# Optimization experiments

Measured on AMD Instinct MI355X. Metric: run time of the kernel, lower is better.

## Reference

```python
import math
import jax, jax.numpy as jnp
import numpy as np

# dims (match init_kwargs / input_specs)
N_H = 16        # heads
N_I = 64        # number of intent slots appended to the key axis
N_B = 8         # buckets (one-hot has N_B+1 classes)
D_MODEL = 1024
D_K = D_MODEL // N_H
EPSILON = 0.25
TOP_K = int(N_I * EPSILON)   # = 16
BS = 2
MAXLEN = 1024
N2 = MAXLEN + N_I            # intent length = seq keys + intents


def setup_inputs() -> dict:
    key = jax.random.key(0)
    k0, k1, k2, k3, k4, k5 = jax.random.split(key, 6)
    item = jax.random.normal(k0, (BS, MAXLEN, D_MODEL), dtype=jnp.float32)
    intent = jax.random.normal(k1, (BS, N2, D_MODEL), dtype=jnp.float32)
    mask = jnp.ones((BS, 1, MAXLEN, N2), dtype=jnp.bool_)
    b_seq = jax.random.randint(k2, (BS, MAXLEN), 0, N_B + 1)
    b_seq2 = jax.random.randint(k3, (BS, N2), 0, N_B + 1)
    # learned params: [1, n_b+1, d_model, h, d_k] and [2, n_b+1, d_model, h, d_k]
    W_item = jax.random.normal(k4, (1, N_B + 1, D_MODEL, N_H, D_K), dtype=jnp.float32) * 0.02
    W_intent = jax.random.normal(k5, (2, N_B + 1, D_MODEL, N_H, D_K), dtype=jnp.float32) * 0.02
    return {"item": item, "intent": intent, "mask": mask,
            "b_seq": b_seq, "b_seq2": b_seq2,
            "W_item": W_item, "W_intent": W_intent}


def _rank_mask(x, k):
    # torch double-sort trick: True where element is NOT among the top-k of the row
    order = jnp.argsort(-x, axis=-1)          # descending sort indices (idx1)
    rank = jnp.argsort(order, axis=-1)        # rank of each position (idx2)
    return rank >= k


def reference(item, intent, mask, b_seq, b_seq2, W_item, W_intent):
    oh_q = jax.nn.one_hot(b_seq, N_B + 1, dtype=item.dtype)      # [b, n, B]
    oh_kv = jax.nn.one_hot(b_seq2, N_B + 1, dtype=intent.dtype)  # [b, m, B]
    # bucket-gated projections
    q = jnp.einsum('bnd,Bdhk,bnB->bhnk', item, W_item[0], oh_q)
    k = jnp.einsum('bmd,Bdhk,bmB->bhmk', intent, W_intent[0], oh_kv)
    v = jnp.einsum('bmd,Bdhk,bmB->bhmk', intent, W_intent[1], oh_kv)
    # attention scores [b, h, n, m]
    scores = jnp.einsum('bhnk,bhmk->bhnm', q, k) / math.sqrt(D_K)
    scores = jnp.where(mask, scores, jnp.float32(-1e30))
    p = jax.nn.softmax(scores, axis=-1)  # dropout = identity (eval reference)
    # split key axis: sequence part vs last n_i intents, top-k mask each part
    p_bs = p[..., :-N_I]
    p_ba = p[..., -N_I:]
    topk_mask = jnp.concatenate([_rank_mask(p_bs, TOP_K), _rank_mask(p_ba, TOP_K)], axis=-1)
    p_masked = jnp.where(topk_mask, jnp.float32(0.0), p)
    # 'belong' indices: argmax position per query row at head 0
    sIdx = jnp.argmax(p_bs[:, 0], axis=-1)[..., None]  # [b, n, 1]
    aIdx = jnp.argmax(p_ba[:, 0], axis=-1)[..., None]  # [b, n, 1]
    x = jnp.einsum('bhnm,bhmk->bhnk', p_masked, v)
    x = jnp.transpose(x, (0, 2, 1, 3)).reshape(BS, MAXLEN, N_H * D_K)
    return (x, sIdx, aIdx)
```

## Files before the change

### kernel.cpp

```cpp
#include <hip/hip_runtime.h>

#define NHEAD   16
#define DK      64
#define DMODEL  1024
#define BSZ     2
#define SEQLEN  1024
#define NI      64
#define NN2     1088
#define NBUCK   9
#define TOPK    16

#define T_ITEM  (BSZ*SEQLEN)
#define T_INT   (BSZ*NN2)

#define Q_OFF   ((size_t)0)
#define K_OFF   (Q_OFF + (size_t)T_ITEM*DMODEL*4)
#define V_OFF   (K_OFF + (size_t)T_INT*DMODEL*4)
#define QKV_BYTES (V_OFF + (size_t)T_INT*DMODEL*4)
#define CNT_OFF QKV_BYTES
#define LI_OFF  (CNT_OFF + 128)
#define LN_OFF  (LI_OFF + (size_t)NBUCK*T_ITEM*4)
#define WS_NEED (LN_OFF + (size_t)NBUCK*T_INT*4)
#define P_OFF   ((WS_NEED + 255) & ~(size_t)255)
#define WS_NEED2 (P_OFF + QKV_BYTES)

#define Q0D_OFF V_OFF
#define K0D_OFF (V_OFF + (size_t)T_ITEM*64*8)

#define X_OUT_ELEMS ((size_t)BSZ*SEQLEN*DMODEL)
#define SIDX_ELEMS  ((size_t)BSZ*SEQLEN)

__device__ __forceinline__ int clampi(int v, int lo, int hi) {
  return v < lo ? lo : (v > hi ? hi : v);
}

__global__ void bucketize_kernel(const int* __restrict__ b_seq, const int* __restrict__ b_seq2,
                                 int* __restrict__ cnt, int* __restrict__ list_item,
                                 int* __restrict__ list_int) {
  int t = blockIdx.x * blockDim.x + threadIdx.x;
  if (t < T_ITEM) {
    int B = clampi(b_seq[t], 0, NBUCK - 1);
    int p = atomicAdd(&cnt[B], 1);
    if (p >= 0 && p < T_ITEM) list_item[B * T_ITEM + p] = t;
  }
  if (t < T_INT) {
    int B = clampi(b_seq2[t], 0, NBUCK - 1);
    int p = atomicAdd(&cnt[NBUCK + B], 1);
    if (p >= 0 && p < T_INT) list_int[B * T_INT + p] = t;
  }
}

__global__ __launch_bounds__(256) void proj_head0_f64_v2(
    const float* __restrict__ item, const float* __restrict__ intent,
    const float* __restrict__ Wq, const float* __restrict__ Wk,
    const int* __restrict__ b_seq, const int* __restrict__ b_seq2,
    double* __restrict__ q0d, double* __restrict__ k0dT) {
  const int blk = blockIdx.x;
  const int wv = (int)threadIdx.x >> 6, lane = (int)threadIdx.x & 63;
  const float* X; const float* W; const int* bs; int tok; bool tr;
  if (blk < T_ITEM) { tok = blk;          X = item;   W = Wq; bs = b_seq;  tr = false; }
  else              { tok = blk - T_ITEM; X = intent; W = Wk; bs = b_seq2; tr = true; }
  const int B = clampi(bs[tok], 0, NBUCK - 1);
  const float* xr = X + (size_t)tok * DMODEL;
  const float* wb = W + (size_t)B * DMODEL * (NHEAD * DK) + lane;
  double acc = 0.0;
  const int d0 = wv * 256;
  #pragma unroll 8
  for (int d = d0; d < d0 + 256; ++d)
    acc += (double)xr[d] * (double)wb[(size_t)d * (NHEAD * DK)];
  __shared__ double part[4][64];
  part[wv][lane] = acc;
  __syncthreads();
  if (wv == 0) {
    double s = ((part[0][lane] + part[1][lane]) + part[2][lane]) + part[3][lane];
    if (tr) k0dT[(size_t)lane * T_INT + tok] = s;
    else    q0d[(size_t)tok * 64 + lane] = s;
  }
}

#define AR 4
__global__ __launch_bounds__(256) void argmax_f64_v2(
    const double* __restrict__ Q0, const double* __restrict__ K0T,
    float* __restrict__ out_s, float* __restrict__ out_a) {
  const int n0 = blockIdx.x * AR;
  const int b = n0 >> 10;
  const int t = (int)threadIdx.x;
  __shared__ double qs[AR][64];
  qs[t >> 6][t & 63] = Q0[(size_t)(n0 + (t >> 6)) * 64 + (t & 63)];
  __syncthreads();
  double v1[AR], v2[AR]; int i1[AR], i2[AR];
  #pragma unroll
  for (int r = 0; r < AR; ++r) {
    v1[r] = -1e300; i1[r] = 0x7FFFFFFF;
    v2[r] = -1e300; i2[r] = 0x7FFFFFFF;
  }
  for (int m = t; m < NN2; m += 256) {
    const double* base = K0T + (size_t)b * NN2 + m;
    double s0 = 0.0, s1 = 0.0, s2 = 0.0, s3 = 0.0;
    #pragma unroll 8
    for (int k = 0; k < 64; ++k) {
      const double kv = base[(size_t)k * T_INT];
      s0 += qs[0][k] * kv; s1 += qs[1][k] * kv;
      s2 += qs[2][k] * kv; s3 += qs[3][k] * kv;
    }
    const double ss[AR] = {s0, s1, s2, s3};
    #pragma unroll
    for (int r = 0; r < AR; ++r) {
      const double s = ss[r];
      if (m < 1024) { if (s > v1[r] || (s == v1[r] && m < i1[r])) { v1[r] = s; i1[r] = m; } }
      else          { if (s > v2[r] || (s == v2[r] && m < i2[r])) { v2[r] = s; i2[r] = m; } }
    }
  }
  __shared__ double bval[256];  __shared__ int bidx[256];
  __shared__ double bval2[256]; __shared__ int bidx2[256];
  for (int r = 0; r < AR; ++r) {
    __syncthreads();
    bval[t] = v1[r]; bidx[t] = i1[r]; bval2[t] = v2[r]; bidx2[t] = i2[r];
    __syncthreads();
    for (int off = 128; off >= 1; off >>= 1) {
      if (t < off) {
        if (bval[t+off] >  bval[t] || (bval[t+off] ==  bval[t] &&  bidx[t+off] <  bidx[t])) { bval[t]  = bval[t+off];  bidx[t]  = bidx[t+off]; }
        if (bval2[t+off] > bval2[t] || (bval2[t+off] == bval2[t] && bidx2[t+off] < bidx2[t])) { bval2[t] = bval2[t+off]; bidx2[t] = bidx2[t+off]; }
      }
      __syncthreads();
    }
    if (t == 0) {
      out_s[n0 + r] = (float)bidx[0];
      out_a[n0 + r] = (float)(bidx2[0] - 1024);
    }
  }
}

#define GTM 128
#define GTN 128
#define GBK 16

__global__ __launch_bounds__(256) void gemm_grouped_fused(
    const float* __restrict__ item, const float* __restrict__ intent,
    const float* __restrict__ Wq, const float* __restrict__ Wk,
    const float* __restrict__ Wv,
    const int* __restrict__ list_item, const int* __restrict__ list_int,
    const int* __restrict__ cnt,
    float* __restrict__ qb, float* __restrict__ kb, float* __restrict__ vb,
    float* __restrict__ pq, float* __restrict__ pk, float* __restrict__ pv,
    const int klen) {
  const int z = blockIdx.z;
  const int s = z / 27;
  const int rem = z - s * 27;
  const int g = rem / 9, B = rem - g * 9;
  const int kbeg = s * klen;
  const float* X;  const float* W;  const int* list;  float* Y;  int n, Tmax;
  if (g == 0)      { X = item;   W = Wq; list = list_item; Y = s ? pq : qb; n = min(cnt[B], T_ITEM);        Tmax = T_ITEM; }
  else if (g == 1) { X = intent; W = Wk; list = list_int;  Y = s ? pk : kb; n = min(cnt[NBUCK + B], T_INT); Tmax = T_INT; }
  else             { X = intent; W = Wv; list = list_int;  Y = s ? pv : vb; n = min(cnt[NBUCK + B], T_INT); Tmax = T_INT; }

  const int row0 = blockIdx.y * GTM;
  if (row0 >= n) return;
  const int rows = min(GTM, n - row0);
  const int c0 = blockIdx.x * GTN;
  const int t = (int)threadIdx.x;

  __shared__ float Xs[GBK][GTM + 4];
  __shared__ float Ws[GBK][GTN];

  const int tokA = t >> 1;
  const int kqA  = (t & 1) * 8;
  const int liA  = clampi(list[row0 + min(tokA, rows - 1)], 0, Tmax - 1);
  const float* xrow = X + (size_t)liA * DMODEL;
  const int kW  = t >> 4;
  const int cW  = (t & 15) * 4;
  const float* wbase = W + ((size_t)B * DMODEL + kW) * (size_t)(NHEAD * DK) + c0 + cW;

  const int ty = t >> 4;
  const int tx = t & 15;

  float acc[8][8];
  #pragma unroll
  for (int i = 0; i < 8; ++i)
    #pragma unroll
    for (int j = 0; j < 8; ++j) acc[i][j] = 0.f;

  float4 xa = *(const float4*)(xrow + kbeg + kqA);
  float4 xb = *(const float4*)(xrow + kbeg + kqA + 4);
  float4 wa = *(const float4*)(wbase + (size_t)kbeg * (NHEAD * DK));
  float4 wc = *(const float4*)(wbase + (size_t)kbeg * (NHEAD * DK) + 64);

  for (int k0 = kbeg; k0 < kbeg + klen; k0 += GBK) {
    __syncthreads();
    Xs[kqA + 0][tokA] = xa.x; Xs[kqA + 1][tokA] = xa.y;
    Xs[kqA + 2][tokA] = xa.z; Xs[kqA + 3][tokA] = xa.w;
    Xs[kqA + 4][tokA] = xb.x; Xs[kqA + 5][tokA] = xb.y;
    Xs[kqA + 6][tokA] = xb.z; Xs[kqA + 7][tokA] = xb.w;
    *(float4*)&Ws[kW][cW]      = wa;
    *(float4*)&Ws[kW][cW + 64] = wc;
    __syncthreads();

    if (k0 + GBK < kbeg + klen) {
      xa = *(const float4*)(xrow + k0 + GBK + kqA);
      xb = *(const float4*)(xrow + k0 + GBK + kqA + 4);
      wa = *(const float4*)(wbase + (size_t)(k0 + GBK) * (NHEAD * DK));
      wc = *(const float4*)(wbase + (size_t)(k0 + GBK) * (NHEAD * DK) + 64);
    }

    #pragma unroll
    for (int kk = 0; kk < GBK; ++kk) {
      float a[8], bv[8];
      *(float4*)&a[0]  = *(const float4*)&Xs[kk][ty * 8];
      *(float4*)&a[4]  = *(const float4*)&Xs[kk][ty * 8 + 4];
      *(float4*)&bv[0] = *(const float4*)&Ws[kk][tx * 4];
      *(float4*)&bv[4] = *(const float4*)&Ws[kk][tx * 4 + 64];
      #pragma unroll
      for (int i = 0; i < 8; ++i)
        #pragma unroll
        for (int j = 0; j < 8; ++j)
          acc[i][j] = fmaf(a[i], bv[j], acc[i][j]);
    }
  }

  #pragma unroll
  for (int i = 0; i < 8; ++i) {
    const int r = ty * 8 + i;
    if (r < rows) {
      const int tok = clampi(list[row0 + r], 0, Tmax - 1);
      float* yr = Y + (size_t)tok * (size_t)(NHEAD * DK) + c0 + tx * 4;
      *(float4*)yr        = make_float4(acc[i][0], acc[i][1], acc[i][2], acc[i][3]);
      *(float4*)(yr + 64) = make_float4(acc[i][4], acc[i][5], acc[i][6], acc[i][7]);
    }
  }
}

__global__ __launch_bounds__(256) void reduce_add(
    float4* __restrict__ y, const float4* __restrict__ p, const int n4) {
  const int stride = gridDim.x * blockDim.x;
  for (int i = blockIdx.x * blockDim.x + threadIdx.x; i < n4; i += stride) {
    float4 a = y[i]; const float4 b = p[i];
    a.x += b.x; a.y += b.y; a.z += b.z; a.w += b.w;
    y[i] = a;
  }
}

__device__ __forceinline__ unsigned ordf(float v) {
  unsigned s = __float_as_uint(v);
  return s ^ ((unsigned)((int)s >> 31) | 0x80000000u);
}
__device__ __forceinline__ float unordf(unsigned u) {
  unsigned s = (u & 0x80000000u) ? (u ^ 0x80000000u) : ~u;
  return __uint_as_float(s);
}
__device__ __forceinline__ unsigned long long shfl_xor_u64(unsigned long long w, int off) {
  unsigned lo = __shfl_xor((unsigned)w, off);
  unsigned hi = __shfl_xor((unsigned)(w >> 32), off);
  return ((unsigned long long)hi << 32) | lo;
}

__global__ __launch_bounds__(256) void attn_kernel(
    const float* __restrict__ Q, const float* __restrict__ K,
    const float* __restrict__ V, float* __restrict__ outx) {
  const int b = blockIdx.z, h = blockIdx.y;
  const int n0 = blockIdx.x * 16;
  const int t = (int)threadIdx.x;
  const int wave = t >> 6, lane = t & 63;

  __shared__ float Qs[16][64];
  __shared__ float Ks[192][68];
  __shared__ int   kept_m[16][32];
  __shared__ float kept_p[16][32];

  {
    const int r = t >> 4, k4 = (t & 15) * 4;
    *(float4*)&Qs[r][k4] =
        *(const float4*)(Q + (size_t)(b * SEQLEN + n0 + r) * (NHEAD * DK) + h * DK + k4);
  }
  __syncthreads();

  const int r0 = wave * 4;
  float sv[4][17];

  #pragma unroll
  for (int p = 0; p < 5; ++p) {
    if (p > 0) __syncthreads();
    #pragma unroll
    for (int j = 0; j < 12; ++j) {
      const int row = (t >> 4) + 16 * j;
      const int k4 = (t & 15) * 4;
      *(float4*)&Ks[row][k4] =
          *(const float4*)(K + (size_t)(b * NN2 + p * 192 + row) * (NHEAD * DK) + h * DK + k4);
    }
    __syncthreads();

    float a0[3], a1[3], a2[3], a3[3];
    #pragma unroll
    for (int c = 0; c < 3; ++c) { a0[c] = 0.f; a1[c] = 0.f; a2[c] = 0.f; a3[c] = 0.f; }
    #pragma unroll 4
    for (int k4 = 0; k4 < 64; k4 += 4) {
      float4 kc[3];
      kc[0] = *(const float4*)&Ks[lane][k4];
      kc[1] = *(const float4*)&Ks[64 + lane][k4];
      kc[2] = *(const float4*)&Ks[128 + lane][k4];
      const float4 q0 = *(const float4*)&Qs[r0 + 0][k4];
      const float4 q1 = *(const float4*)&Qs[r0 + 1][k4];
      const float4 q2 = *(const float4*)&Qs[r0 + 2][k4];
      const float4 q3 = *(const float4*)&Qs[r0 + 3][k4];
      #pragma unroll
      for (int c = 0; c < 3; ++c) {
        a0[c] = fmaf(q0.x, kc[c].x, a0[c]); a0[c] = fmaf(q0.y, kc[c].y, a0[c]);
        a0[c] = fmaf(q0.z, kc[c].z, a0[c]); a0[c] = fmaf(q0.w, kc[c].w, a0[c]);
        a1[c] = fmaf(q1.x, kc[c].x, a1[c]); a1[c] = fmaf(q1.y, kc[c].y, a1[c]);
        a1[c] = fmaf(q1.z, kc[c].z, a1[c]); a1[c] = fmaf(q1.w, kc[c].w, a1[c]);
        a2[c] = fmaf(q2.x, kc[c].x, a2[c]); a2[c] = fmaf(q2.y, kc[c].y, a2[c]);
        a2[c] = fmaf(q2.z, kc[c].z, a2[c]); a2[c] = fmaf(q2.w, kc[c].w, a2[c]);
        a3[c] = fmaf(q3.x, kc[c].x, a3[c]); a3[c] = fmaf(q3.y, kc[c].y, a3[c]);
        a3[c] = fmaf(q3.z, kc[c].z, a3[c]); a3[c] = fmaf(q3.w, kc[c].w, a3[c]);
      }
    }
    #pragma unroll
    for (int c = 0; c < 3; ++c) {
      sv[0][3 * p + c] = a0[c] * 0.125f; sv[1][3 * p + c] = a1[c] * 0.125f;
      sv[2][3 * p + c] = a2[c] * 0.125f; sv[3][3 * p + c] = a3[c] * 0.125f;
    }
  }

  {
    __syncthreads();
    #pragma unroll
    for (int j = 0; j < 8; ++j) {
      const int row = (t >> 4) + 16 * j;
      const int k4 = (t & 15) * 4;
      *(float4*)&Ks[row][k4] =
          *(const float4*)(K + (size_t)(b * NN2 + 960 + row) * (NHEAD * DK) + h * DK + k4);
    }
    __syncthreads();

    float a0[2], a1[2], a2[2], a3[2];
    #pragma unroll
    for (int c = 0; c < 2; ++c) { a0[c] = 0.f; a1[c] = 0.f; a2[c] = 0.f; a3[c] = 0.f; }
    #pragma unroll 4
    for (int k4 = 0; k4 < 64; k4 += 4) {
      float4 kc[2];
      kc[0] = *(const float4*)&Ks[lane][k4];
      kc[1] = *(const float4*)&Ks[64 + lane][k4];
      const float4 q0 = *(const float4*)&Qs[r0 + 0][k4];
      const float4 q1 = *(const float4*)&Qs[r0 + 1][k4];
      const float4 q2 = *(const float4*)&Qs[r0 + 2][k4];
      const float4 q3 = *(const float4*)&Qs[r0 + 3][k4];
      #pragma unroll
      for (int c = 0; c < 2; ++c) {
        a0[c] = fmaf(q0.x, kc[c].x, a0[c]); a0[c] = fmaf(q0.y, kc[c].y, a0[c]);
        a0[c] = fmaf(q0.z, kc[c].z, a0[c]); a0[c] = fmaf(q0.w, kc[c].w, a0[c]);
        a1[c] = fmaf(q1.x, kc[c].x, a1[c]); a1[c] = fmaf(q1.y, kc[c].y, a1[c]);
        a1[c] = fmaf(q1.z, kc[c].z, a1[c]); a1[c] = fmaf(q1.w, kc[c].w, a1[c]);
        a2[c] = fmaf(q2.x, kc[c].x, a2[c]); a2[c] = fmaf(q2.y, kc[c].y, a2[c]);
        a2[c] = fmaf(q2.z, kc[c].z, a2[c]); a2[c] = fmaf(q2.w, kc[c].w, a2[c]);
        a3[c] = fmaf(q3.x, kc[c].x, a3[c]); a3[c] = fmaf(q3.y, kc[c].y, a3[c]);
        a3[c] = fmaf(q3.z, kc[c].z, a3[c]); a3[c] = fmaf(q3.w, kc[c].w, a3[c]);
      }
    }
    #pragma unroll
    for (int c = 0; c < 2; ++c) {
      sv[0][15 + c] = a0[c] * 0.125f; sv[1][15 + c] = a1[c] * 0.125f;
      sv[2][15 + c] = a2[c] * 0.125f; sv[3][15 + c] = a3[c] * 0.125f;
    }
  }

  float M_[4], invL_[4];
  {
    float L_[4];
    #pragma unroll
    for (int r = 0; r < 4; ++r) {
      float M = -3.402823466e38f;
      #pragma unroll
      for (int c = 0; c < 17; ++c) M = fmaxf(M, sv[r][c]);
      M_[r] = M;
    }
    #pragma unroll
    for (int off = 32; off >= 1; off >>= 1) {
      #pragma unroll
      for (int r = 0; r < 4; ++r) M_[r] = fmaxf(M_[r], __shfl_xor(M_[r], off));
    }
    #pragma unroll
    for (int r = 0; r < 4; ++r) {
      float L = 0.f;
      #pragma unroll
      for (int c = 0; c < 17; ++c) L += __expf(sv[r][c] - M_[r]);
      L_[r] = L;
    }
    #pragma unroll
    for (int off = 32; off >= 1; off >>= 1) {
      #pragma unroll
      for (int r = 0; r < 4; ++r) L_[r] += __shfl_xor(L_[r], off);
    }
    #pragma unroll
    for (int r = 0; r < 4; ++r) invL_[r] = 1.0f / L_[r];
  }

  unsigned kh[4][16];
  #pragma unroll
  for (int r = 0; r < 4; ++r)
    #pragma unroll
    for (int c = 0; c < 16; ++c) kh[r][c] = ordf(sv[r][c]);

  unsigned long long b1_[4], b2_[4];
  unsigned alive_[4];
  #pragma unroll
  for (int r = 0; r < 4; ++r) {
    unsigned long long b1 = 0ull, b2 = 0ull;
    #pragma unroll
    for (int c = 0; c < 16; ++c) {
      const unsigned long long k64 =
          ((unsigned long long)kh[r][c] << 32) | (unsigned)~(unsigned)(c * 64 + lane);
      const unsigned long long mn = (k64 < b1) ? k64 : b1;
      b1 = (k64 > b1) ? k64 : b1;
      b2 = (mn > b2) ? mn : b2;
    }
    b1_[r] = b1; b2_[r] = b2; alive_[r] = 0xFFFFu;
  }

  for (int round = 0; round < TOPK; ++round) {
    unsigned long long w0 = b1_[0], w1 = b1_[1], w2 = b1_[2], w3 = b1_[3];
    #pragma unroll
    for (int off = 1; off < 64; off <<= 1) {
      unsigned long long o;
      o = shfl_xor_u64(w0, off); w0 = (o > w0) ? o : w0;
      o = shfl_xor_u64(w1, off); w1 = (o > w1) ? o : w1;
      o = shfl_xor_u64(w2, off); w2 = (o > w2) ? o : w2;
      o = shfl_xor_u64(w3, off); w3 = (o > w3) ? o : w3;
    }
    const unsigned long long ws[4] = {w0, w1, w2, w3};
    #pragma unroll
    for (int r = 0; r < 4; ++r) {
      const unsigned long long w = ws[r];
      const int m = (int)((~(unsigned)w) & 1023u);
      if (lane == round) {
        kept_m[r0 + r][round] = m;
        kept_p[r0 + r][round] = __expf(unordf((unsigned)(w >> 32)) - M_[r]) * invL_[r];
      }
      if ((m & 63) == lane) {
        alive_[r] &= ~(1u << (m >> 6));
        if (b2_[r]) { b1_[r] = b2_[r]; b2_[r] = 0ull; }
        else {
          unsigned long long mx = 0ull;
          #pragma unroll
          for (int c = 0; c < 16; ++c) {
            const unsigned long long k64 =
                ((unsigned long long)kh[r][c] << 32) | (unsigned)~(unsigned)(c * 64 + lane);
            if ((alive_[r] >> c) & 1u) mx = (k64 > mx) ? k64 : mx;
          }
          b1_[r] = mx;
        }
      }
    }
  }

  {
    unsigned long long w_[4];
    #pragma unroll
    for (int r = 0; r < 4; ++r)
      w_[r] = ((unsigned long long)ordf(sv[r][16]) << 32) | (unsigned)~(unsigned)lane;
    #pragma unroll
    for (int k = 2; k <= 64; k <<= 1) {
      #pragma unroll
      for (int j = k >> 1; j >= 1; j >>= 1) {
        const bool tm = (((lane & j) != 0) == ((lane & k) != 0));
        #pragma unroll
        for (int r = 0; r < 4; ++r) {
          const unsigned long long o = shfl_xor_u64(w_[r], j);
          w_[r] = ((o > w_[r]) == tm) ? o : w_[r];
        }
      }
    }
    if (lane < TOPK) {
      #pragma unroll
      for (int r = 0; r < 4; ++r) {
        kept_m[r0 + r][TOPK + lane] = 1024 + (int)((~(unsigned)w_[r]) & 63u);
        kept_p[r0 + r][TOPK + lane] =
            __expf(unordf((unsigned)(w_[r] >> 32)) - M_[r]) * invL_[r];
      }
    }
  }
  __syncthreads();

  #pragma unroll
  for (int rr = 0; rr < 4; ++rr) {
    const int r_loc = wave * 4 + rr;
    const int n = n0 + r_loc;
    float x = 0.f;
    #pragma unroll
    for (int i = 0; i < 32; ++i) {
      const int m = clampi(kept_m[r_loc][i], 0, NN2 - 1);
      const float p = kept_p[r_loc][i];
      x = fmaf(p, V[(size_t)(b * NN2 + m) * (NHEAD * DK) + h * DK + lane], x);
    }
    outx[(size_t)(b * SEQLEN + n) * (NHEAD * DK) + h * DK + lane] = x;
  }
}

extern "C" void kernel_launch(void* const* d_in, const int* in_sizes, int n_in,
                              void* d_out, int out_size, void* d_ws, size_t ws_size,
                              hipStream_t stream) {
  const float* item    = (const float*)d_in[0];
  const float* intent  = (const float*)d_in[1];
  const int*   b_seq   = (const int*)d_in[3];
  const int*   b_seq2  = (const int*)d_in[4];
  const float* W_item  = (const float*)d_in[5];
  const float* W_int   = (const float*)d_in[6];

  if (ws_size < WS_NEED) return;

  char* ws = (char*)d_ws;
  float* qb = (float*)(ws + Q_OFF);
  float* kb = (float*)(ws + K_OFF);
  float* vb = (float*)(ws + V_OFF);
  double* q0d = (double*)(ws + Q0D_OFF);
  double* k0dT = (double*)(ws + K0D_OFF);
  int* cnt       = (int*)(ws + CNT_OFF);
  int* list_item = (int*)(ws + LI_OFF);
  int* list_int  = (int*)(ws + LN_OFF);

  const bool sk = (ws_size >= WS_NEED2);
  float* pq = sk ? (float*)(ws + P_OFF + Q_OFF) : qb;
  float* pk = sk ? (float*)(ws + P_OFF + K_OFF) : kb;
  float* pv = sk ? (float*)(ws + P_OFF + V_OFF) : vb;

  float* outx  = (float*)d_out;
  float* out_s = outx + X_OUT_ELEMS;
  float* out_a = out_s + SIDX_ELEMS;

  hipMemsetAsync(cnt, 0, 128, stream);
  bucketize_kernel<<<dim3(9), 256, 0, stream>>>(b_seq, b_seq2, cnt, list_item, list_int);

  proj_head0_f64_v2<<<dim3(T_ITEM + T_INT), 256, 0, stream>>>(
      item, intent, W_item, W_int, b_seq, b_seq2, q0d, k0dT);
  argmax_f64_v2<<<dim3(T_ITEM / AR), 256, 0, stream>>>(q0d, k0dT, out_s, out_a);

  const int klen = sk ? (DMODEL / 2) : DMODEL;
  const int nz   = sk ? 54 : 27;
  gemm_grouped_fused<<<dim3((NHEAD * DK) / GTN, 17, nz), 256, 0, stream>>>(
      item, intent,
      W_item, W_int, W_int + (size_t)NBUCK * DMODEL * (NHEAD * DK),
      list_item, list_int, cnt, qb, kb, vb, pq, pk, pv, klen);
  if (sk) {
    reduce_add<<<dim3(2048), 256, 0, stream>>>(
        (float4*)(ws + Q_OFF), (float4*)(ws + P_OFF), (int)(QKV_BYTES / 16));
  }

  attn_kernel<<<dim3(SEQLEN / 16, NHEAD, BSZ), 256, 0, stream>>>(qb, kb, vb, outx);
}
```

Before: 691.8 us.

## Merge bucketize into head-0 projection launch and register-prefetch K tiles in attention

The bucketize kernel becomes the first 9 blocks of the head-0 f64 projection launch, which removes one kernel launch. The two pieces of work are independent, so merging them is safe. In the attention kernel, the next 192-row K tile is now loaded into registers (12 float4 per thread) while the current tile is being computed, so global-load latency overlaps the FMA loop. The cost is about 48 extra VGPRs per thread, which may lower occupancy.

```diff
diff --git a/kernel.cpp b/kernel.cpp
--- a/kernel.cpp
+++ b/kernel.cpp
@@ -34,32 +34,32 @@
   return v < lo ? lo : (v > hi ? hi : v);
 }
 
-__global__ void bucketize_kernel(const int* __restrict__ b_seq, const int* __restrict__ b_seq2,
-                                 int* __restrict__ cnt, int* __restrict__ list_item,
-                                 int* __restrict__ list_int) {
-  int t = blockIdx.x * blockDim.x + threadIdx.x;
-  if (t < T_ITEM) {
-    int B = clampi(b_seq[t], 0, NBUCK - 1);
-    int p = atomicAdd(&cnt[B], 1);
-    if (p >= 0 && p < T_ITEM) list_item[B * T_ITEM + p] = t;
-  }
-  if (t < T_INT) {
-    int B = clampi(b_seq2[t], 0, NBUCK - 1);
-    int p = atomicAdd(&cnt[NBUCK + B], 1);
-    if (p >= 0 && p < T_INT) list_int[B * T_INT + p] = t;
-  }
-}
-
-__global__ __launch_bounds__(256) void proj_head0_f64_v2(
+__global__ __launch_bounds__(256) void bucketize_proj(
+    const int* __restrict__ b_seq, const int* __restrict__ b_seq2,
+    int* __restrict__ cnt, int* __restrict__ list_item, int* __restrict__ list_int,
     const float* __restrict__ item, const float* __restrict__ intent,
     const float* __restrict__ Wq, const float* __restrict__ Wk,
-    const int* __restrict__ b_seq, const int* __restrict__ b_seq2,
     double* __restrict__ q0d, double* __restrict__ k0dT) {
   const int blk = blockIdx.x;
+  if (blk < 9) {
+    int t = blk * blockDim.x + threadIdx.x;
+    if (t < T_ITEM) {
+      int B = clampi(b_seq[t], 0, NBUCK - 1);
+      int p = atomicAdd(&cnt[B], 1);
+      if (p >= 0 && p < T_ITEM) list_item[B * T_ITEM + p] = t;
+    }
+    if (t < T_INT) {
+      int B = clampi(b_seq2[t], 0, NBUCK - 1);
+      int p = atomicAdd(&cnt[NBUCK + B], 1);
+      if (p >= 0 && p < T_INT) list_int[B * T_INT + p] = t;
+    }
+    return;
+  }
+  const int pblk = blk - 9;
   const int wv = (int)threadIdx.x >> 6, lane = (int)threadIdx.x & 63;
   const float* X; const float* W; const int* bs; int tok; bool tr;
-  if (blk < T_ITEM) { tok = blk;          X = item;   W = Wq; bs = b_seq;  tr = false; }
-  else              { tok = blk - T_ITEM; X = intent; W = Wk; bs = b_seq2; tr = true; }
+  if (pblk < T_ITEM) { tok = pblk;          X = item;   W = Wq; bs = b_seq;  tr = false; }
+  else               { tok = pblk - T_ITEM; X = intent; W = Wk; bs = b_seq2; tr = true; }
   const int B = clampi(bs[tok], 0, NBUCK - 1);
   const float* xr = X + (size_t)tok * DMODEL;
   const float* wb = W + (size_t)B * DMODEL * (NHEAD * DK) + lane;
@@ -266,11 +266,15 @@
   __shared__ int   kept_m[16][32];
   __shared__ float kept_p[16][32];
 
-  {
-    const int r = t >> 4, k4 = (t & 15) * 4;
-    *(float4*)&Qs[r][k4] =
-        *(const float4*)(Q + (size_t)(b * SEQLEN + n0 + r) * (NHEAD * DK) + h * DK + k4);
-  }
+  const int rS = t >> 4;
+  const int k4S = (t & 15) * 4;
+
+  float4 pf[12];
+  #pragma unroll
+  for (int j = 0; j < 12; ++j)
+    pf[j] = *(const float4*)(K + (size_t)(b * NN2 + rS + 16 * j) * (NHEAD * DK) + h * DK + k4S);
+  *(float4*)&Qs[rS][k4S] =
+      *(const float4*)(Q + (size_t)(b * SEQLEN + n0 + rS) * (NHEAD * DK) + h * DK + k4S);
   __syncthreads();
 
   const int r0 = wave * 4;
@@ -280,13 +284,19 @@
   for (int p = 0; p < 5; ++p) {
     if (p > 0) __syncthreads();
     #pragma unroll
-    for (int j = 0; j < 12; ++j) {
-      const int row = (t >> 4) + 16 * j;
-      const int k4 = (t & 15) * 4;
-      *(float4*)&Ks[row][k4] =
-          *(const float4*)(K + (size_t)(b * NN2 + p * 192 + row) * (NHEAD * DK) + h * DK + k4);
-    }
-    __syncthreads();
+    for (int j = 0; j < 12; ++j)
+      *(float4*)&Ks[rS + 16 * j][k4S] = pf[j];
+    __syncthreads();
+
+    if (p < 4) {
+      #pragma unroll
+      for (int j = 0; j < 12; ++j)
+        pf[j] = *(const float4*)(K + (size_t)(b * NN2 + (p + 1) * 192 + rS + 16 * j) * (NHEAD * DK) + h * DK + k4S);
+    } else {
+      #pragma unroll
+      for (int j = 0; j < 8; ++j)
+        pf[j] = *(const float4*)(K + (size_t)(b * NN2 + 960 + rS + 16 * j) * (NHEAD * DK) + h * DK + k4S);
+    }
 
     float a0[3], a1[3], a2[3], a3[3];
     #pragma unroll
@@ -323,12 +333,8 @@
   {
     __syncthreads();
     #pragma unroll
-    for (int j = 0; j < 8; ++j) {
-      const int row = (t >> 4) + 16 * j;
-      const int k4 = (t & 15) * 4;
-      *(float4*)&Ks[row][k4] =
-          *(const float4*)(K + (size_t)(b * NN2 + 960 + row) * (NHEAD * DK) + h * DK + k4);
-    }
+    for (int j = 0; j < 8; ++j)
+      *(float4*)&Ks[rS + 16 * j][k4S] = pf[j];
     __syncthreads();
 
     float a0[2], a1[2], a2[2], a3[2];
@@ -526,10 +532,10 @@
   float* out_a = out_s + SIDX_ELEMS;
 
   hipMemsetAsync(cnt, 0, 128, stream);
-  bucketize_kernel<<<dim3(9), 256, 0, stream>>>(b_seq, b_seq2, cnt, list_item, list_int);
-
-  proj_head0_f64_v2<<<dim3(T_ITEM + T_INT), 256, 0, stream>>>(
-      item, intent, W_item, W_int, b_seq, b_seq2, q0d, k0dT);
+
+  bucketize_proj<<<dim3(9 + T_ITEM + T_INT), 256, 0, stream>>>(
+      b_seq, b_seq2, cnt, list_item, list_int,
+      item, intent, W_item, W_int, q0d, k0dT);
   argmax_f64_v2<<<dim3(T_ITEM / AR), 256, 0, stream>>>(q0d, k0dT, out_s, out_a);
 
   const int klen = sk ? (DMODEL / 2) : DMODEL;
```

After: 728.2 us. 1.05x slower.
